# Kernel optimization log

Hardware: AMD Instinct MI355X
Metric: run time of the kernel (lower is better)

## Reference

```python
import jax, jax.numpy as jnp
import numpy as np

VOCAB = 50000
EMB = 300
HID = 300
LAYERS = 2
NTAGS = 11  # tags 0..8 are real labels, 9=START, 10=STOP
START = NTAGS - 2
STOP = NTAGS - 1
NEG = -10000.0


def _lstm_params(key, in_dim, hid):
    k = 1.0 / np.sqrt(hid)
    ks = jax.random.split(key, 4)
    u = lambda kk, shp: jax.random.uniform(kk, shp, jnp.float32, -k, k)
    return {
        'Wi': u(ks[0], (4 * hid, in_dim)),
        'Wh': u(ks[1], (4 * hid, hid)),
        'bi': u(ks[2], (4 * hid,)),
        'bh': u(ks[3], (4 * hid,)),
    }


def _run_lstm(p, xs, reverse=False):
    # xs: [T, B, D] -> [T, B, H]
    B = xs.shape[1]
    H = p['Wh'].shape[1]
    pre = jnp.einsum('tbd,gd->tbg', xs, p['Wi']) + p['bi'] + p['bh']

    def step(carry, pre_t):
        h, c = carry
        g = pre_t + h @ p['Wh'].T
        i, f, gg, o = jnp.split(g, 4, axis=-1)
        i = jax.nn.sigmoid(i)
        f = jax.nn.sigmoid(f)
        gg = jnp.tanh(gg)
        o = jax.nn.sigmoid(o)
        c = f * c + i * gg
        h = o * jnp.tanh(c)
        return (h, c), h

    init = (jnp.zeros((B, H), xs.dtype), jnp.zeros((B, H), xs.dtype))
    _, hs = jax.lax.scan(step, init, pre, reverse=reverse)
    return hs


def setup_inputs() -> dict:
    key = jax.random.key(0)
    ks = jax.random.split(key, 12)
    x = jax.random.randint(ks[0], (64, 512), 0, VOCAB, dtype=jnp.int32)
    emb = jax.random.normal(ks[1], (VOCAB, EMB), jnp.float32) * 0.02
    lstm = []
    ki = 2
    for layer in range(LAYERS):
        in_dim = EMB if layer == 0 else 2 * HID
        fwd = _lstm_params(ks[ki], in_dim, HID); ki += 1
        bwd = _lstm_params(ks[ki], in_dim, HID); ki += 1
        lstm.append((fwd, bwd))
    Wout = jax.random.normal(ks[ki], (NTAGS, 2 * HID), jnp.float32) * 0.02
    bout = jnp.zeros((NTAGS,), jnp.float32)
    trans = jax.random.normal(ks[ki + 1], (NTAGS, NTAGS), jnp.float32) * 0.1
    # transitions[i, j] = score of transitioning TO i FROM j
    trans = trans.at[START, :].set(NEG).at[:, STOP].set(NEG)
    params = {'emb': emb, 'Wout': Wout, 'bout': bout, 'trans': trans}
    for li, (f, b) in enumerate(lstm):
        for nm, d in (('f', f), ('b', b)):
            for k2, v in d.items():
                params[f'l{li}{nm}_{k2}'] = v
    return {'x': x, **params}


def _features(x, params):
    h = params['emb'][x]  # [B,T,E]
    h = jnp.transpose(h, (1, 0, 2))  # [T,B,E]
    for li in range(LAYERS):
        pf = {k2: params[f'l{li}f_{k2}'] for k2 in ('Wi', 'Wh', 'bi', 'bh')}
        pb = {k2: params[f'l{li}b_{k2}'] for k2 in ('Wi', 'Wh', 'bi', 'bh')}
        hf = _run_lstm(pf, h)
        hb = _run_lstm(pb, h, reverse=True)
        h = jnp.concatenate([hf, hb], axis=-1)  # [T,B,2H]
    feats = jnp.einsum('tbh,gh->tbg', h, params['Wout']) + params['bout']
    return feats  # [T,B,NTAGS]


def _viterbi(feats, trans):
    # feats: [T,B,K]; trans[i,j]: to i from j
    T, B, K = feats.shape
    init = jnp.full((B, K), NEG, feats.dtype).at[:, START].set(0.0)

    def step(fv, feat_t):
        # scores[b, i, j] = fv[b, j] + trans[i, j]
        scores = fv[:, None, :] + trans[None, :, :]
        bp = jnp.argmax(scores, axis=-1)  # [B,K]
        fv_new = jnp.max(scores, axis=-1) + feat_t
        return fv_new, bp

    fv, bps = jax.lax.scan(step, init, feats)  # bps: [T,B,K]
    term = fv + trans[STOP][None, :]
    best_last = jnp.argmax(term, axis=-1)  # [B]
    path_score = jnp.max(term, axis=-1)

    def back(tag, bp_t):
        prev = jnp.take_along_axis(bp_t, tag[:, None], axis=-1)[:, 0]
        return prev, tag

    _, path = jax.lax.scan(back, best_last, bps, reverse=True)  # [T,B]
    return path_score, jnp.transpose(path)  # [B], [B,T]


def reference(x, emb, Wout, bout, trans,
              l0f_Wi, l0f_Wh, l0f_bi, l0f_bh, l0b_Wi, l0b_Wh, l0b_bi, l0b_bh,
              l1f_Wi, l1f_Wh, l1f_bi, l1f_bh, l1b_Wi, l1b_Wh, l1b_bi, l1b_bh):
    params = dict(emb=emb, Wout=Wout, bout=bout, trans=trans,
                  l0f_Wi=l0f_Wi, l0f_Wh=l0f_Wh, l0f_bi=l0f_bi, l0f_bh=l0f_bh,
                  l0b_Wi=l0b_Wi, l0b_Wh=l0b_Wh, l0b_bi=l0b_bi, l0b_bh=l0b_bh,
                  l1f_Wi=l1f_Wi, l1f_Wh=l1f_Wh, l1f_bi=l1f_bi, l1f_bh=l1f_bh,
                  l1b_Wi=l1b_Wi, l1b_Wh=l1b_Wh, l1b_bi=l1b_bi, l1b_bh=l1b_bh)
    feats = _features(x, params)
    path_score, path = _viterbi(feats, trans)
    return path_score, path
```

## Files before the change

### kernel.cpp

```cpp
#include <hip/hip_runtime.h>
#include <hip/hip_bf16.h>

#define T_SEQ 512
#define NBATCH 64
#define HID 300
#define G4 1200
#define NTAG 11
#define TAG_START 9
#define TAG_STOP 10
#define NEGV -10000.0f
#define NWGD 38
#define NKT 10
#define HXE (40*2*64*8)
#define NPREW 150
#define FLGS 16
#define FLGN 152
#define FLGDIR (FLGN*FLGS)

typedef unsigned short u16;
using short8 = __attribute__((ext_vector_type(8))) short;
using f32x4  = __attribute__((ext_vector_type(4))) float;
using i32x4  = __attribute__((ext_vector_type(4))) int;

#define MF(a, b, c) __builtin_amdgcn_mfma_f32_16x16x32_bf16((a), (b), (c), 0, 0, 0)

__device__ __forceinline__ float sigf(float x) { return 1.0f / (1.0f + expf(-x)); }

__device__ __forceinline__ u16 f2bf(float x) {
    unsigned u = __float_as_uint(x);
    unsigned r = (u + 0x7FFFu + ((u >> 16) & 1u)) >> 16;
    return (u16)r;
}
__device__ __forceinline__ float bf2f(u16 h) {
    return __uint_as_float((unsigned)h << 16);
}

__device__ __forceinline__ i32x4 ld_cc_x4(const u16* p) {
    i32x4 r;
    asm volatile("global_load_dwordx4 %0, %1, off sc0 sc1" : "=v"(r) : "v"(p) : "memory");
    return r;
}
__device__ __forceinline__ unsigned ld_cc_b32(const unsigned* p) {
    unsigned r;
    asm volatile("global_load_dword %0, %1, off sc0 sc1\n\t"
                 "s_waitcnt vmcnt(0)" : "=v"(r) : "v"(p) : "memory");
    return r;
}
__device__ __forceinline__ void st_cc_x4(u16* p, i32x4 v) {
    asm volatile("global_store_dwordx4 %0, %1, off sc0 sc1" :: "v"(p), "v"(v) : "memory");
}
__device__ __forceinline__ void st_cc_b32(unsigned* p, unsigned v) {
    asm volatile("global_store_dword %0, %1, off sc0 sc1" :: "v"(p), "v"(v) : "memory");
}
__device__ __forceinline__ void wait_vm0() {
    asm volatile("s_waitcnt vmcnt(0)" ::: "memory");
}

__global__ __launch_bounds__(256) void k_gather(const int* __restrict__ x,
                                                const float* __restrict__ emb,
                                                u16* __restrict__ xs0)
{
    int t = blockIdx.x;
    __shared__ int rid[NBATCH];
    if (threadIdx.x < NBATCH) rid[threadIdx.x] = x[threadIdx.x * T_SEQ + t];
    __syncthreads();
    for (int o = threadIdx.x; o < 64 * 40; o += 256) {
        int b = o / 40, m8 = o - b * 40;
        unsigned hw[4], lw[4];
#pragma unroll
        for (int p = 0; p < 4; ++p) {
            int k0 = m8 * 8 + p * 2;
            float v0 = (k0 < 300)     ? emb[(size_t)rid[b] * 300 + k0]     : 0.0f;
            float v1 = (k0 + 1 < 300) ? emb[(size_t)rid[b] * 300 + k0 + 1] : 0.0f;
            u16 h0 = f2bf(v0), h1 = f2bf(v1);
            u16 l0 = f2bf(v0 - bf2f(h0)), l1 = f2bf(v1 - bf2f(h1));
            hw[p] = (unsigned)h0 | ((unsigned)h1 << 16);
            lw[p] = (unsigned)l0 | ((unsigned)l1 << 16);
        }
        u16* dst = xs0 + (((size_t)t * 40 + m8) * 64 + b) * 16;
        *(i32x4*)dst       = i32x4{(int)hw[0], (int)hw[1], (int)hw[2], (int)hw[3]};
        *(i32x4*)(dst + 8) = i32x4{(int)lw[0], (int)lw[1], (int)lw[2], (int)lw[3]};
    }
}

__global__ __launch_bounds__(256) void k_zpad(u16* __restrict__ xs1)
{
    int t = blockIdx.x;
    i32x4* base = (i32x4*)(xs1 + (((size_t)t * 80 + 76) * 64) * 16);
    i32x4 z = {0, 0, 0, 0};
    for (int o = threadIdx.x; o < 4 * 64 * 2; o += 256) base[o] = z;
}

template<int KT, int KMAX>
__device__ __forceinline__ void pregemm_role(
    const u16* __restrict__ xs,
    const float* __restrict__ Wi, const float* __restrict__ bi, const float* __restrict__ bh,
    float* __restrict__ pre, int jtile, int dir, int t0f, int t0b, int s0, int s1, int tid)
{
    int w = tid >> 6, l = tid & 63;
    int hh = l >> 4, kbx = l >> 4;
    int jj = jtile * 4 + hh;
    int bcol = w * 16 + (l & 15);

    short8 aH[KT], aL[KT];
    {
        int r = l & 15;
        int g = r & 3, uo = r >> 2;
        const float* wr = Wi + ((size_t)g * 300 + jtile * 4 + uo) * KMAX;
        int kb0 = kbx * 8;
#pragma unroll
        for (int kt = 0; kt < KT; ++kt) {
            short8 vh, vl;
#pragma unroll
            for (int e = 0; e < 8; ++e) {
                int kp = kt * 32 + kb0 + e;
                bool valid; int cc;
                if (KMAX == 600) { valid = (kp < 300) || (kp >= 304 && kp < 604); cc = (kp < 300) ? kp : kp - 4; }
                else             { valid = (kp < 300); cc = kp; }
                float wv = valid ? wr[cc] : 0.0f;
                u16 hb = f2bf(wv);
                vh[e] = (short)hb;
                vl[e] = (short)f2bf(wv - bf2f(hb));
            }
            aH[kt] = vh; aL[kt] = vl;
        }
    }
    float bias[4];
#pragma unroll
    for (int q = 0; q < 4; ++q) bias[q] = bi[q * 300 + jj] + bh[q * 300 + jj];

    const int NB8 = KT * 4;
    for (int s = s0; s < s1; ++s) {
        int t = dir ? (t0b - s) : (t0f + s);
        f32x4 a0 = {0.f,0.f,0.f,0.f}, a1 = {0.f,0.f,0.f,0.f}, a2 = {0.f,0.f,0.f,0.f};
#pragma unroll
        for (int kt = 0; kt < KT; ++kt) {
            const u16* gx = xs + (((size_t)t * NB8 + (4 * kt + kbx)) * 64 + bcol) * 16;
            short8 bhv = *(const short8*)gx;
            short8 blv = *(const short8*)(gx + 8);
            a0 = MF(aH[kt], bhv, a0);
            a1 = MF(aL[kt], bhv, a1);
            a2 = MF(aH[kt], blv, a2);
        }
#pragma unroll
        for (int q = 0; q < 4; ++q)
            pre[((size_t)s * G4 + q * 300 + jj) * 64 + bcol] = a0[q] + a1[q] + a2[q] + bias[q];
    }
}

template<int KT, int KMAX>
__global__ __launch_bounds__(256) void k_pregemm(
    const u16* __restrict__ xs,
    const float* __restrict__ WiF, const float* __restrict__ WiB,
    const float* __restrict__ biF, const float* __restrict__ bhF,
    const float* __restrict__ biB, const float* __restrict__ bhB,
    float* __restrict__ preF, float* __restrict__ preB,
    int t0f, int t0b, int NSL, int C)
{
    int bx = blockIdx.x;
    int idx = bx / (2 * NSL);
    int rem = bx - idx * 2 * NSL;
    int sl = rem >> 1, dir = rem & 1;
    int s0 = sl * 32, s1 = min(s0 + 32, C);
    pregemm_role<KT, KMAX>(xs,
        dir ? WiB : WiF, dir ? biB : biF, dir ? bhB : bhF,
        dir ? preB : preF, idx, dir, t0f, t0b, s0, s1, threadIdx.x);
}

template<int MODE>
__device__ __forceinline__ void lstm_role(
    const float* __restrict__ preF, const float* __restrict__ preB,
    const float* __restrict__ WhF, const float* __restrict__ WhB,
    u16* __restrict__ hx, float* __restrict__ cbuf,
    float* __restrict__ xs2, u16* __restrict__ xs1,
    int t0f, int t0b, int C, int first,
    unsigned* __restrict__ flags,
    volatile unsigned* wgprog,
    int bid, int tid)
{
    __builtin_amdgcn_s_setprio(1);
    int dir = bid & 1, idx = bid >> 1;
    const float* pre = dir ? preB : preF;
    const float* Wh  = dir ? WhB : WhF;
    u16* hxd = hx + (size_t)dir * 2 * HXE;
    float* cb = cbuf + (size_t)dir * 300 * 64;
    unsigned* flg = flags + (size_t)dir * FLGDIR;
    int w = tid >> 6, l = tid & 63;
    int hh = l >> 4, kbx = l >> 4;
    int bcol = w * 16 + (l & 15);
    int j0 = idx * 8;
    int ju0 = j0 + hh, ju1 = j0 + 4 + hh;
    int jc0 = min(ju0, 299), jc1 = min(ju1, 299);
    bool jv0 = ju0 < 300, jv1 = ju1 < 300;

    unsigned* myflag = flg + (size_t)(idx * 4 + w) * FLGS;
    const unsigned* shardp = flg + (size_t)(w * 38 + min(l, 37)) * FLGS;
    bool shact = l < 38;

    if (l == 0) wgprog[w] = 0;
    __syncthreads();

    short8 aH[2][NKT], aL[2][NKT];
    {
        int r = l & 15;
        int g = r & 3, uo = r >> 2;
#pragma unroll
        for (int q = 0; q < 2; ++q) {
            int jr = j0 + q * 4 + uo;
            const float* wr = Wh + ((size_t)g * 300 + min(jr, 299)) * 300;
            bool jvr = jr < 300;
#pragma unroll
            for (int kt = 0; kt < NKT; ++kt) {
                short8 vh, vl;
#pragma unroll
                for (int e = 0; e < 8; ++e) {
                    int k = kt * 32 + kbx * 8 + e;
                    float wv = (jvr && k < 300) ? wr[k] : 0.0f;
                    u16 hb = f2bf(wv);
                    vh[e] = (short)hb;
                    vl[e] = (short)f2bf(wv - bf2f(hb));
                }
                aH[q][kt] = vh; aL[q][kt] = vl;
            }
        }
    }
    float c0 = first ? 0.0f : cb[(size_t)jc0 * 64 + bcol];
    float c1 = first ? 0.0f : cb[(size_t)jc1 * 64 + bcol];

    float p0[4], p1[4];
#pragma unroll
    for (int g = 0; g < 4; ++g) {
        p0[g] = pre[((size_t)g * 300 + jc0) * 64 + bcol];
        p1[g] = pre[((size_t)g * 300 + jc1) * 64 + bcol];
    }

    int pp = 0;
    for (int s = 0; s < C; ++s) {
        f32x4 aA0 = {0.f,0.f,0.f,0.f}, aB0 = {0.f,0.f,0.f,0.f}, aC0 = {0.f,0.f,0.f,0.f};
        f32x4 aA1 = {0.f,0.f,0.f,0.f}, aB1 = {0.f,0.f,0.f,0.f}, aC1 = {0.f,0.f,0.f,0.f};
        if (!(first && s == 0)) {
            const u16* hxr = hxd + (size_t)pp * HXE;
            i32x4 bh[NKT], bl[NKT];
#pragma unroll
            for (int kt = 0; kt < NKT; ++kt) {
                const u16* gp = hxr + (size_t)(4 * kt + kbx) * 1024 + (size_t)bcol * 8;
                bh[kt] = ld_cc_x4(gp);
            }
#pragma unroll
            for (int kt = 0; kt < NKT; ++kt) {
                const u16* gp = hxr + (size_t)(4 * kt + kbx) * 1024 + (size_t)bcol * 8;
                bl[kt] = ld_cc_x4(gp + 512);
            }
            asm volatile("s_waitcnt vmcnt(10)" ::: "memory");
            __builtin_amdgcn_sched_barrier(0);
#pragma unroll
            for (int kt = 0; kt < NKT; ++kt) {
                short8 bhv = __builtin_bit_cast(short8, bh[kt]);
                aA0 = MF(aH[0][kt], bhv, aA0);
                aB0 = MF(aL[0][kt], bhv, aB0);
                aA1 = MF(aH[1][kt], bhv, aA1);
                aB1 = MF(aL[1][kt], bhv, aB1);
            }
            wait_vm0();
            __builtin_amdgcn_sched_barrier(0);
#pragma unroll
            for (int kt = 0; kt < NKT; ++kt) {
                short8 blv = __builtin_bit_cast(short8, bl[kt]);
                aC0 = MF(aH[0][kt], blv, aC0);
                aC1 = MF(aH[1][kt], blv, aC1);
            }
        }
        float hv0, hv1;
        {
            float gi = sigf(aA0[0] + aB0[0] + aC0[0] + p0[0]);
            float gf = sigf(aA0[1] + aB0[1] + aC0[1] + p0[1]);
            float gg = tanhf(aA0[2] + aB0[2] + aC0[2] + p0[2]);
            float go = sigf(aA0[3] + aB0[3] + aC0[3] + p0[3]);
            c0 = gf * c0 + gi * gg;
            hv0 = go * tanhf(c0);
            if (!jv0) hv0 = 0.0f;
        }
        {
            float gi = sigf(aA1[0] + aB1[0] + aC1[0] + p1[0]);
            float gf = sigf(aA1[1] + aB1[1] + aC1[1] + p1[1]);
            float gg = tanhf(aA1[2] + aB1[2] + aC1[2] + p1[2]);
            float go = sigf(aA1[3] + aB1[3] + aC1[3] + p1[3]);
            c1 = gf * c1 + gi * gg;
            hv1 = go * tanhf(c1);
            if (!jv1) hv1 = 0.0f;
        }
        u16 hb0 = f2bf(hv0);
        unsigned pk0 = (unsigned)hb0 | ((unsigned)f2bf(hv0 - bf2f(hb0)) << 16);
        u16 hb1 = f2bf(hv1);
        unsigned pk1 = (unsigned)hb1 | ((unsigned)f2bf(hv1 - bf2f(hb1)) << 16);
        int ls = l & 15;
        unsigned a0 = __shfl(pk0, ls), a1 = __shfl(pk0, ls + 16), a2 = __shfl(pk0, ls + 32), a3 = __shfl(pk0, ls + 48);
        unsigned b0 = __shfl(pk1, ls), b1 = __shfl(pk1, ls + 16), b2 = __shfl(pk1, ls + 32), b3 = __shfl(pk1, ls + 48);
        i32x4 hi4 = {(int)((a0 & 0xffffu) | (a1 << 16)), (int)((a2 & 0xffffu) | (a3 << 16)),
                     (int)((b0 & 0xffffu) | (b1 << 16)), (int)((b2 & 0xffffu) | (b3 << 16))};
        i32x4 lo4 = {(int)((a0 >> 16) | (a1 & 0xffff0000u)), (int)((a2 >> 16) | (a3 & 0xffff0000u)),
                     (int)((b0 >> 16) | (b1 & 0xffff0000u)), (int)((b2 >> 16) | (b3 & 0xffff0000u))};
        int t = dir ? (t0b - s) : (t0f + s);
        if (l < 16) {
            int b = w * 16 + l;
            u16* hxw = hxd + (size_t)(pp ^ 1) * HXE + (size_t)idx * 1024 + (size_t)b * 8;
            st_cc_x4(hxw, hi4);
            st_cc_x4(hxw + 512, lo4);
        }
        wait_vm0();
        if (l == 0) st_cc_b32(myflag, (unsigned)(s + 1));
        if (MODE == 0) {
            if (jv0) xs2[((size_t)t * 600 + dir * 300 + ju0) * 64 + bcol] = hv0;
            if (jv1) xs2[((size_t)t * 600 + dir * 300 + ju1) * 64 + bcol] = hv1;
        } else if (l < 16) {
            int b = w * 16 + l;
            u16* xd = xs1 + (((size_t)t * 80 + dir * 38 + idx) * 64 + b) * 16;
            *(i32x4*)xd       = hi4;
            *(i32x4*)(xd + 8) = lo4;
        }
        if (s + 1 < C) {
#pragma unroll
            for (int g = 0; g < 4; ++g) {
                p0[g] = pre[((size_t)(s + 1) * G4 + (size_t)g * 300 + jc0) * 64 + bcol];
                p1[g] = pre[((size_t)(s + 1) * G4 + (size_t)g * 300 + jc1) * 64 + bcol];
            }
            unsigned tgt = (unsigned)(s + 1);
            unsigned ok;
            do {
                unsigned v = tgt;
                if (shact) v = ld_cc_b32(shardp);
                ok = (v >= tgt) ? 1u : 0u;
            } while (!__all(ok));
            if (l == 0) wgprog[w] = tgt;
            while (!(wgprog[0] >= tgt && wgprog[1] >= tgt &&
                     wgprog[2] >= tgt && wgprog[3] >= tgt)) {
                __builtin_amdgcn_s_sleep(1);
            }
        }
        pp ^= 1;
    }
    if (jv0) cb[(size_t)jc0 * 64 + bcol] = c0;
    if (jv1) cb[(size_t)jc1 * 64 + bcol] = c1;
}

template<int KT, int KMAX, int MODE>
__global__ __launch_bounds__(256, 1) void k_chunk(
    const u16* __restrict__ xsN,
    const float* __restrict__ WiF, const float* __restrict__ WiB,
    const float* __restrict__ biF, const float* __restrict__ bhF,
    const float* __restrict__ biB, const float* __restrict__ bhB,
    float* __restrict__ preNF, float* __restrict__ preNB,
    int t0fN, int t0bN, int do_pre, int CN,
    const float* __restrict__ preF, const float* __restrict__ preB,
    const float* __restrict__ WhF, const float* __restrict__ WhB,
    u16* __restrict__ hx, float* __restrict__ cbuf,
    float* __restrict__ xs2, u16* __restrict__ xs1,
    int t0f, int t0b, int C, int first,
    unsigned* __restrict__ flags)
{
    __shared__ unsigned wgprog[4];
    int bid = blockIdx.x;
    if (bid < 2 * NWGD) {
        lstm_role<MODE>(preF, preB, WhF, WhB, hx, cbuf, xs2, xs1,
                        t0f, t0b, C, first, flags, wgprog, bid, threadIdx.x);
    } else if (do_pre) {
        int wg = bid - 2 * NWGD;
        int jtile = wg >> 1, dir = wg & 1;
        pregemm_role<KT, KMAX>(xsN,
            dir ? WiB : WiF, dir ? biB : biF, dir ? bhB : bhF,
            dir ? preNB : preNF, jtile, dir, t0fN, t0bN, 0, CN, threadIdx.x);
    }
}

__global__ __launch_bounds__(256) void k_feats(
    const float* __restrict__ xs2, const float* __restrict__ Wout,
    const float* __restrict__ bout, float* __restrict__ feats)
{
    int t = blockIdx.x;
    int tid = threadIdx.x;
    int b = tid & 63, g0 = tid >> 6;
    const float* xa = xs2 + (size_t)t * 600 * 64 + b;
    for (int g = g0; g < NTAG; g += 4) {
        float acc = bout[g];
        const float* wr = Wout + (size_t)g * 600;
#pragma unroll 4
        for (int k = 0; k < 600; ++k) acc += wr[k] * xa[(size_t)k * 64];
        feats[((size_t)t * NTAG + g) * 64 + b] = acc;
    }
}

__global__ __launch_bounds__(256) void k_viterbi(
    const float* __restrict__ feats, const float* __restrict__ trans,
    float* __restrict__ out)
{
    __shared__ unsigned char bp[4][T_SEQ * NTAG];
    int tid = threadIdx.x;
    int wv = tid >> 6, lane = tid & 63;
    int b = blockIdx.x * 4 + wv;
    int i = (lane < NTAG) ? lane : 0;
    bool act = lane < NTAG;
    float trow[NTAG];
#pragma unroll
    for (int j = 0; j < NTAG; ++j) trow[j] = trans[i * NTAG + j];
    float fv = (lane == TAG_START) ? 0.0f : NEGV;
    for (int t = 0; t < T_SEQ; ++t) {
        float m = -3.0e38f; int arg = 0;
#pragma unroll
        for (int j = 0; j < NTAG; ++j) {
            float fvj = __shfl(fv, j, 64);
            float sc = fvj + trow[j];
            if (sc > m) { m = sc; arg = j; }
        }
        float ft = feats[((size_t)t * NTAG + i) * 64 + b];
        fv = m + ft;
        if (act) bp[wv][t * NTAG + lane] = (unsigned char)arg;
    }
    float term = act ? (fv + trans[TAG_STOP * NTAG + i]) : -3.0e38f;
    int bi_ = lane;
#pragma unroll
    for (int off = 32; off >= 1; off >>= 1) {
        float ov = __shfl_xor(term, off, 64);
        int oi = __shfl_xor(bi_, off, 64);
        if (ov > term || (ov == term && oi < bi_)) { term = ov; bi_ = oi; }
    }
    if (lane == 0) {
        out[b] = term;
        int tag = bi_;
        float* po = out + 64 + (size_t)b * T_SEQ;
        for (int t = T_SEQ - 1; t >= 0; --t) {
            po[t] = (float)tag;
            tag = bp[wv][t * NTAG + tag];
        }
    }
}

extern "C" void kernel_launch(void* const* d_in, const int* in_sizes, int n_in,
                              void* d_out, int out_size, void* d_ws, size_t ws_size,
                              hipStream_t stream)
{
    (void)in_sizes; (void)n_in; (void)out_size;
    const int*   x     = (const int*)d_in[0];
    const float* emb   = (const float*)d_in[1];
    const float* Wout  = (const float*)d_in[2];
    const float* bout  = (const float*)d_in[3];
    const float* trans = (const float*)d_in[4];

    float* ws = (float*)d_ws;
    const size_t XS2F = (size_t)T_SEQ * 600 * NBATCH;
    const size_t XS1U = (size_t)T_SEQ * 80 * 64 * 16;
    const size_t FEA  = (size_t)T_SEQ * NTAG * NBATCH;

    float* xs2 = ws;
    u16* xs0 = (u16*)ws;
    u16* xs1 = (u16*)(ws + XS2F);
    float* featB = (float*)(xs1 + XS1U);
    float* cB = featB + FEA;
    u16* hxB = (u16*)(cB + 2 * 300 * 64);
    unsigned* flagsB = (unsigned*)(hxB + 4 * HXE);
    unsigned* padB = flagsB + 64ULL * 2 * FLGDIR;
    float* preBase = (float*)(padB + 16);
    size_t fixedBytes = (size_t)((char*)preBase - (char*)ws);

    int Cmax = 512;
    while (Cmax > 16 && fixedBytes + 4ULL * Cmax * G4 * NBATCH * 4ULL > ws_size) Cmax >>= 1;
    size_t slotF = 2ULL * Cmax * G4 * NBATCH;
    float* preS[2] = { preBase, preBase + slotF };

    int sizes[40], off[41], nch = 0;
    {
        int rem = T_SEQ;
        int f = (Cmax >= 64) ? 32 : Cmax;
        sizes[nch++] = f; rem -= f;
        while (rem > 0) { int s = rem < Cmax ? rem : Cmax; sizes[nch++] = s; rem -= s; }
        off[0] = 0;
        for (int i = 0; i < nch; ++i) off[i + 1] = off[i] + sizes[i];
    }

    (void)hipMemsetAsync(hxB, 0,
        4 * HXE * sizeof(u16) + (64ULL * 2 * FLGDIR) * sizeof(unsigned), stream);
    k_gather<<<T_SEQ, 256, 0, stream>>>(x, emb, xs0);
    k_zpad<<<T_SEQ, 256, 0, stream>>>(xs1);

    for (int layer = 0; layer < 2; ++layer) {
        int base = 5 + layer * 8;
        const float* WiF = (const float*)d_in[base + 0];
        const float* WhF = (const float*)d_in[base + 1];
        const float* biF = (const float*)d_in[base + 2];
        const float* bhF = (const float*)d_in[base + 3];
        const float* WiB = (const float*)d_in[base + 4];
        const float* WhB = (const float*)d_in[base + 5];
        const float* biB = (const float*)d_in[base + 6];
        const float* bhB = (const float*)d_in[base + 7];

        int NSL0 = (sizes[0] + 31) / 32;
        if (layer == 0)
            k_pregemm<10, 300><<<75 * 2 * NSL0, 256, 0, stream>>>(
                xs0, WiF, WiB, biF, bhF, biB, bhB,
                preS[0], preS[0] + slotF / 2, 0, T_SEQ - 1, NSL0, sizes[0]);
        else
            k_pregemm<20, 600><<<75 * 2 * NSL0, 256, 0, stream>>>(
                xs1, WiF, WiB, biF, bhF, biB, bhB,
                preS[0], preS[0] + slotF / 2, 0, T_SEQ - 1, NSL0, sizes[0]);

        for (int ci = 0; ci < nch; ++ci) {
            int cur = ci & 1, nxt = cur ^ 1;
            int t0f = off[ci], t0b = (T_SEQ - 1) - off[ci];
            int do_pre = (ci + 1 < nch) ? 1 : 0;
            int CN = do_pre ? sizes[ci + 1] : 0;
            int t0fN = off[ci + 1], t0bN = (T_SEQ - 1) - off[ci + 1];
            int slot = layer * 32 + ci;
            unsigned* flags = flagsB + (size_t)slot * 2 * FLGDIR;
            if (layer == 0)
                k_chunk<10, 300, 1><<<2 * NWGD + NPREW, 256, 0, stream>>>(
                    xs0, WiF, WiB, biF, bhF, biB, bhB,
                    preS[nxt], preS[nxt] + slotF / 2, t0fN, t0bN, do_pre, CN,
                    preS[cur], preS[cur] + slotF / 2, WhF, WhB, hxB, cB,
                    xs2, xs1, t0f, t0b, sizes[ci], (ci == 0) ? 1 : 0, flags);
            else
                k_chunk<20, 600, 0><<<2 * NWGD + NPREW, 256, 0, stream>>>(
                    xs1, WiF, WiB, biF, bhF, biB, bhB,
                    preS[nxt], preS[nxt] + slotF / 2, t0fN, t0bN, do_pre, CN,
                    preS[cur], preS[cur] + slotF / 2, WhF, WhB, hxB, cB,
                    xs2, xs1, t0f, t0b, sizes[ci], (ci == 0) ? 1 : 0, flags);
        }
    }
    k_feats<<<T_SEQ, 256, 0, stream>>>(xs2, Wout, bout, featB);
    k_viterbi<<<16, 256, 0, stream>>>(featB, trans, (float*)d_out);
}
```

Before: 5.896 ms.

## Halve recurrent LSTM workgroups, give each 16 hidden units, keep low-bf16 weights in LDS

Each direction's recurrent LSTM now runs on 19 workgroups instead of 38, and each workgroup owns 16 hidden units instead of 8. The high bf16 half of the recurrent weights stays in registers, while the low half moves into a 40KB LDS buffer that the MFMA loop reads each step. This cuts the number of workgroups that take part in the per-timestep cross-workgroup flag synchronisation and frees compute units for the overlapped pre-GEMM. In exchange each workgroup does twice the MFMA and activation work per step, and LDS reads are added to the critical path.

```diff
diff --git a/kernel.cpp b/kernel.cpp
--- a/kernel.cpp
+++ b/kernel.cpp
@@ -9,12 +9,12 @@
 #define TAG_START 9
 #define TAG_STOP 10
 #define NEGV -10000.0f
-#define NWGD 38
+#define NWGD 19
 #define NKT 10
 #define HXE (40*2*64*8)
 #define NPREW 150
 #define FLGS 16
-#define FLGN 152
+#define FLGN 76
 #define FLGDIR (FLGN*FLGS)
 
 typedef unsigned short u16;
@@ -175,7 +175,7 @@
     float* __restrict__ xs2, u16* __restrict__ xs1,
     int t0f, int t0b, int C, int first,
     unsigned* __restrict__ flags,
-    volatile unsigned* wgprog,
+    char* __restrict__ alo, volatile unsigned* wgprog,
     int bid, int tid)
 {
     __builtin_amdgcn_s_setprio(1);
@@ -188,24 +188,27 @@
     int w = tid >> 6, l = tid & 63;
     int hh = l >> 4, kbx = l >> 4;
     int bcol = w * 16 + (l & 15);
-    int j0 = idx * 8;
-    int ju0 = j0 + hh, ju1 = j0 + 4 + hh;
-    int jc0 = min(ju0, 299), jc1 = min(ju1, 299);
-    bool jv0 = ju0 < 300, jv1 = ju1 < 300;
+    int j0 = idx * 16;
+    int blk0 = idx * 2, blk1 = idx * 2 + 1;
+
+    int ju[4], jc[4]; bool jv[4];
+#pragma unroll
+    for (int q = 0; q < 4; ++q) {
+        ju[q] = j0 + q * 4 + hh;
+        jc[q] = min(ju[q], 299);
+        jv[q] = ju[q] < 300;
+    }
 
     unsigned* myflag = flg + (size_t)(idx * 4 + w) * FLGS;
-    const unsigned* shardp = flg + (size_t)(w * 38 + min(l, 37)) * FLGS;
-    bool shact = l < 38;
-
-    if (l == 0) wgprog[w] = 0;
-    __syncthreads();
-
-    short8 aH[2][NKT], aL[2][NKT];
+    const unsigned* shardp = flg + (size_t)(w * 19 + min(l, 18)) * FLGS;
+    bool shact = l < 19;
+
+    short8 aH[4][NKT];
     {
         int r = l & 15;
         int g = r & 3, uo = r >> 2;
 #pragma unroll
-        for (int q = 0; q < 2; ++q) {
+        for (int q = 0; q < 4; ++q) {
             int jr = j0 + q * 4 + uo;
             const float* wr = Wh + ((size_t)g * 300 + min(jr, 299)) * 300;
             bool jvr = jr < 300;
@@ -220,24 +223,30 @@
                     vh[e] = (short)hb;
                     vl[e] = (short)f2bf(wv - bf2f(hb));
                 }
-                aH[q][kt] = vh; aL[q][kt] = vl;
-            }
-        }
-    }
-    float c0 = first ? 0.0f : cb[(size_t)jc0 * 64 + bcol];
-    float c1 = first ? 0.0f : cb[(size_t)jc1 * 64 + bcol];
-
-    float p0[4], p1[4];
-#pragma unroll
-    for (int g = 0; g < 4; ++g) {
-        p0[g] = pre[((size_t)g * 300 + jc0) * 64 + bcol];
-        p1[g] = pre[((size_t)g * 300 + jc1) * 64 + bcol];
-    }
+                aH[q][kt] = vh;
+                if (q == w)
+                    *(short8*)(alo + ((size_t)(q * NKT + kt) * 1024) + (size_t)l * 16) = vl;
+            }
+        }
+    }
+    if (l == 0) wgprog[w] = 0;
+    __syncthreads();
+
+    float c[4];
+#pragma unroll
+    for (int q = 0; q < 4; ++q) c[q] = first ? 0.0f : cb[(size_t)jc[q] * 64 + bcol];
+
+    float p[4][4];
+#pragma unroll
+    for (int q = 0; q < 4; ++q)
+#pragma unroll
+        for (int g = 0; g < 4; ++g)
+            p[q][g] = pre[((size_t)g * 300 + jc[q]) * 64 + bcol];
 
     int pp = 0;
     for (int s = 0; s < C; ++s) {
-        f32x4 aA0 = {0.f,0.f,0.f,0.f}, aB0 = {0.f,0.f,0.f,0.f}, aC0 = {0.f,0.f,0.f,0.f};
-        f32x4 aA1 = {0.f,0.f,0.f,0.f}, aB1 = {0.f,0.f,0.f,0.f}, aC1 = {0.f,0.f,0.f,0.f};
+        f32x4 z = {0.f,0.f,0.f,0.f};
+        f32x4 aA[4] = {z, z, z, z}, aB[4] = {z, z, z, z}, aC[4] = {z, z, z, z};
         if (!(first && s == 0)) {
             const u16* hxr = hxd + (size_t)pp * HXE;
             i32x4 bh[NKT], bl[NKT];
@@ -256,74 +265,79 @@
 #pragma unroll
             for (int kt = 0; kt < NKT; ++kt) {
                 short8 bhv = __builtin_bit_cast(short8, bh[kt]);
-                aA0 = MF(aH[0][kt], bhv, aA0);
-                aB0 = MF(aL[0][kt], bhv, aB0);
-                aA1 = MF(aH[1][kt], bhv, aA1);
-                aB1 = MF(aL[1][kt], bhv, aB1);
+#pragma unroll
+                for (int q = 0; q < 4; ++q)
+                    aA[q] = MF(aH[q][kt], bhv, aA[q]);
+#pragma unroll
+                for (int q = 0; q < 4; ++q) {
+                    short8 alv = *(const short8*)(alo + ((size_t)(q * NKT + kt) * 1024) + (size_t)l * 16);
+                    aB[q] = MF(alv, bhv, aB[q]);
+                }
             }
             wait_vm0();
             __builtin_amdgcn_sched_barrier(0);
 #pragma unroll
             for (int kt = 0; kt < NKT; ++kt) {
                 short8 blv = __builtin_bit_cast(short8, bl[kt]);
-                aC0 = MF(aH[0][kt], blv, aC0);
-                aC1 = MF(aH[1][kt], blv, aC1);
-            }
-        }
-        float hv0, hv1;
-        {
-            float gi = sigf(aA0[0] + aB0[0] + aC0[0] + p0[0]);
-            float gf = sigf(aA0[1] + aB0[1] + aC0[1] + p0[1]);
-            float gg = tanhf(aA0[2] + aB0[2] + aC0[2] + p0[2]);
-            float go = sigf(aA0[3] + aB0[3] + aC0[3] + p0[3]);
-            c0 = gf * c0 + gi * gg;
-            hv0 = go * tanhf(c0);
-            if (!jv0) hv0 = 0.0f;
-        }
-        {
-            float gi = sigf(aA1[0] + aB1[0] + aC1[0] + p1[0]);
-            float gf = sigf(aA1[1] + aB1[1] + aC1[1] + p1[1]);
-            float gg = tanhf(aA1[2] + aB1[2] + aC1[2] + p1[2]);
-            float go = sigf(aA1[3] + aB1[3] + aC1[3] + p1[3]);
-            c1 = gf * c1 + gi * gg;
-            hv1 = go * tanhf(c1);
-            if (!jv1) hv1 = 0.0f;
-        }
-        u16 hb0 = f2bf(hv0);
-        unsigned pk0 = (unsigned)hb0 | ((unsigned)f2bf(hv0 - bf2f(hb0)) << 16);
-        u16 hb1 = f2bf(hv1);
-        unsigned pk1 = (unsigned)hb1 | ((unsigned)f2bf(hv1 - bf2f(hb1)) << 16);
+#pragma unroll
+                for (int q = 0; q < 4; ++q)
+                    aC[q] = MF(aH[q][kt], blv, aC[q]);
+            }
+        }
+        float hv[4]; unsigned pk[4];
+#pragma unroll
+        for (int q = 0; q < 4; ++q) {
+            float gi = sigf(aA[q][0] + aB[q][0] + aC[q][0] + p[q][0]);
+            float gf = sigf(aA[q][1] + aB[q][1] + aC[q][1] + p[q][1]);
+            float gg = tanhf(aA[q][2] + aB[q][2] + aC[q][2] + p[q][2]);
+            float go = sigf(aA[q][3] + aB[q][3] + aC[q][3] + p[q][3]);
+            c[q] = gf * c[q] + gi * gg;
+            float h = go * tanhf(c[q]);
+            if (!jv[q]) h = 0.0f;
+            hv[q] = h;
+            u16 hb = f2bf(h);
+            pk[q] = (unsigned)hb | ((unsigned)f2bf(h - bf2f(hb)) << 16);
+        }
         int ls = l & 15;
-        unsigned a0 = __shfl(pk0, ls), a1 = __shfl(pk0, ls + 16), a2 = __shfl(pk0, ls + 32), a3 = __shfl(pk0, ls + 48);
-        unsigned b0 = __shfl(pk1, ls), b1 = __shfl(pk1, ls + 16), b2 = __shfl(pk1, ls + 32), b3 = __shfl(pk1, ls + 48);
-        i32x4 hi4 = {(int)((a0 & 0xffffu) | (a1 << 16)), (int)((a2 & 0xffffu) | (a3 << 16)),
-                     (int)((b0 & 0xffffu) | (b1 << 16)), (int)((b2 & 0xffffu) | (b3 << 16))};
-        i32x4 lo4 = {(int)((a0 >> 16) | (a1 & 0xffff0000u)), (int)((a2 >> 16) | (a3 & 0xffff0000u)),
-                     (int)((b0 >> 16) | (b1 & 0xffff0000u)), (int)((b2 >> 16) | (b3 & 0xffff0000u))};
+        unsigned q0a = __shfl(pk[0], ls), q0b = __shfl(pk[0], ls + 16), q0c = __shfl(pk[0], ls + 32), q0d = __shfl(pk[0], ls + 48);
+        unsigned q1a = __shfl(pk[1], ls), q1b = __shfl(pk[1], ls + 16), q1c = __shfl(pk[1], ls + 32), q1d = __shfl(pk[1], ls + 48);
+        unsigned q2a = __shfl(pk[2], ls), q2b = __shfl(pk[2], ls + 16), q2c = __shfl(pk[2], ls + 32), q2d = __shfl(pk[2], ls + 48);
+        unsigned q3a = __shfl(pk[3], ls), q3b = __shfl(pk[3], ls + 16), q3c = __shfl(pk[3], ls + 32), q3d = __shfl(pk[3], ls + 48);
+        i32x4 hi4_0 = {(int)((q0a & 0xffffu) | (q0b << 16)), (int)((q0c & 0xffffu) | (q0d << 16)),
+                       (int)((q1a & 0xffffu) | (q1b << 16)), (int)((q1c & 0xffffu) | (q1d << 16))};
+        i32x4 lo4_0 = {(int)((q0a >> 16) | (q0b & 0xffff0000u)), (int)((q0c >> 16) | (q0d & 0xffff0000u)),
+                       (int)((q1a >> 16) | (q1b & 0xffff0000u)), (int)((q1c >> 16) | (q1d & 0xffff0000u))};
+        i32x4 hi4_1 = {(int)((q2a & 0xffffu) | (q2b << 16)), (int)((q2c & 0xffffu) | (q2d << 16)),
+                       (int)((q3a & 0xffffu) | (q3b << 16)), (int)((q3c & 0xffffu) | (q3d << 16))};
+        i32x4 lo4_1 = {(int)((q2a >> 16) | (q2b & 0xffff0000u)), (int)((q2c >> 16) | (q2d & 0xffff0000u)),
+                       (int)((q3a >> 16) | (q3b & 0xffff0000u)), (int)((q3c >> 16) | (q3d & 0xffff0000u))};
         int t = dir ? (t0b - s) : (t0f + s);
-        if (l < 16) {
-            int b = w * 16 + l;
-            u16* hxw = hxd + (size_t)(pp ^ 1) * HXE + (size_t)idx * 1024 + (size_t)b * 8;
-            st_cc_x4(hxw, hi4);
-            st_cc_x4(hxw + 512, lo4);
+        i32x4 h4 = (l < 16) ? hi4_0 : hi4_1;
+        i32x4 l4 = (l < 16) ? lo4_0 : lo4_1;
+        int blkS = (l < 16) ? blk0 : blk1;
+        int bb = w * 16 + ls;
+        if (l < 32) {
+            u16* hxw = hxd + (size_t)(pp ^ 1) * HXE + (size_t)blkS * 1024 + (size_t)bb * 8;
+            st_cc_x4(hxw, h4);
+            st_cc_x4(hxw + 512, l4);
         }
         wait_vm0();
         if (l == 0) st_cc_b32(myflag, (unsigned)(s + 1));
         if (MODE == 0) {
-            if (jv0) xs2[((size_t)t * 600 + dir * 300 + ju0) * 64 + bcol] = hv0;
-            if (jv1) xs2[((size_t)t * 600 + dir * 300 + ju1) * 64 + bcol] = hv1;
-        } else if (l < 16) {
-            int b = w * 16 + l;
-            u16* xd = xs1 + (((size_t)t * 80 + dir * 38 + idx) * 64 + b) * 16;
-            *(i32x4*)xd       = hi4;
-            *(i32x4*)(xd + 8) = lo4;
+#pragma unroll
+            for (int q = 0; q < 4; ++q)
+                if (jv[q]) xs2[((size_t)t * 600 + dir * 300 + ju[q]) * 64 + bcol] = hv[q];
+        } else if (l < 32) {
+            u16* xd = xs1 + (((size_t)t * 80 + dir * 38 + blkS) * 64 + bb) * 16;
+            *(i32x4*)xd       = h4;
+            *(i32x4*)(xd + 8) = l4;
         }
         if (s + 1 < C) {
 #pragma unroll
-            for (int g = 0; g < 4; ++g) {
-                p0[g] = pre[((size_t)(s + 1) * G4 + (size_t)g * 300 + jc0) * 64 + bcol];
-                p1[g] = pre[((size_t)(s + 1) * G4 + (size_t)g * 300 + jc1) * 64 + bcol];
-            }
+            for (int q = 0; q < 4; ++q)
+#pragma unroll
+                for (int g = 0; g < 4; ++g)
+                    p[q][g] = pre[((size_t)(s + 1) * G4 + (size_t)g * 300 + jc[q]) * 64 + bcol];
             unsigned tgt = (unsigned)(s + 1);
             unsigned ok;
             do {
@@ -339,8 +353,9 @@
         }
         pp ^= 1;
     }
-    if (jv0) cb[(size_t)jc0 * 64 + bcol] = c0;
-    if (jv1) cb[(size_t)jc1 * 64 + bcol] = c1;
+#pragma unroll
+    for (int q = 0; q < 4; ++q)
+        if (jv[q]) cb[(size_t)jc[q] * 64 + bcol] = c[q];
 }
 
 template<int KT, int KMAX, int MODE>
@@ -358,11 +373,13 @@
     int t0f, int t0b, int C, int first,
     unsigned* __restrict__ flags)
 {
-    __shared__ unsigned wgprog[4];
+    __shared__ __align__(16) char smem[40 * 1024 + 64];
     int bid = blockIdx.x;
     if (bid < 2 * NWGD) {
         lstm_role<MODE>(preF, preB, WhF, WhB, hx, cbuf, xs2, xs1,
-                        t0f, t0b, C, first, flags, wgprog, bid, threadIdx.x);
+                        t0f, t0b, C, first, flags,
+                        smem, (volatile unsigned*)(smem + 40 * 1024),
+                        bid, threadIdx.x);
     } else if (do_pre) {
         int wg = bid - 2 * NWGD;
         int jtile = wg >> 1, dir = wg & 1;
```

Measured after the change: 7.197 ms. 22.1% more time.

## Split next-chunk input GEMM out of LSTM chunk kernel into separate launch

Applied to the files above, without the earlier changes.

Removes the extra pre-GEMM workgroups that ran alongside the recurrent LSTM workgroups in k_chunk, and instead launches k_pregemm as a separate kernel after each chunk. This undoes the overlap of the next chunk's input projection with the current chunk's recurrence. The aim is to stop the pre-GEMM blocks from competing with the latency-critical recurrent blocks for CUs, cache and memory bandwidth. The cost is that the projection work becomes serialized between chunks.

```diff
diff --git a/kernel.cpp b/kernel.cpp
--- a/kernel.cpp
+++ b/kernel.cpp
@@ -12,7 +12,6 @@
 #define NWGD 38
 #define NKT 10
 #define HXE (40*2*64*8)
-#define NPREW 150
 #define FLGS 16
 #define FLGN 152
 #define FLGDIR (FLGN*FLGS)
@@ -343,14 +342,8 @@
     if (jv1) cb[(size_t)jc1 * 64 + bcol] = c1;
 }
 
-template<int KT, int KMAX, int MODE>
+template<int MODE>
 __global__ __launch_bounds__(256, 1) void k_chunk(
-    const u16* __restrict__ xsN,
-    const float* __restrict__ WiF, const float* __restrict__ WiB,
-    const float* __restrict__ biF, const float* __restrict__ bhF,
-    const float* __restrict__ biB, const float* __restrict__ bhB,
-    float* __restrict__ preNF, float* __restrict__ preNB,
-    int t0fN, int t0bN, int do_pre, int CN,
     const float* __restrict__ preF, const float* __restrict__ preB,
     const float* __restrict__ WhF, const float* __restrict__ WhB,
     u16* __restrict__ hx, float* __restrict__ cbuf,
@@ -359,17 +352,8 @@
     unsigned* __restrict__ flags)
 {
     __shared__ unsigned wgprog[4];
-    int bid = blockIdx.x;
-    if (bid < 2 * NWGD) {
-        lstm_role<MODE>(preF, preB, WhF, WhB, hx, cbuf, xs2, xs1,
-                        t0f, t0b, C, first, flags, wgprog, bid, threadIdx.x);
-    } else if (do_pre) {
-        int wg = bid - 2 * NWGD;
-        int jtile = wg >> 1, dir = wg & 1;
-        pregemm_role<KT, KMAX>(xsN,
-            dir ? WiB : WiF, dir ? biB : biF, dir ? bhB : bhF,
-            dir ? preNB : preNF, jtile, dir, t0fN, t0bN, 0, CN, threadIdx.x);
-    }
+    lstm_role<MODE>(preF, preB, WhF, WhB, hx, cbuf, xs2, xs1,
+                    t0f, t0b, C, first, flags, wgprog, blockIdx.x, threadIdx.x);
 }
 
 __global__ __launch_bounds__(256) void k_feats(
@@ -505,23 +489,30 @@
         for (int ci = 0; ci < nch; ++ci) {
             int cur = ci & 1, nxt = cur ^ 1;
             int t0f = off[ci], t0b = (T_SEQ - 1) - off[ci];
-            int do_pre = (ci + 1 < nch) ? 1 : 0;
-            int CN = do_pre ? sizes[ci + 1] : 0;
-            int t0fN = off[ci + 1], t0bN = (T_SEQ - 1) - off[ci + 1];
             int slot = layer * 32 + ci;
             unsigned* flags = flagsB + (size_t)slot * 2 * FLGDIR;
             if (layer == 0)
-                k_chunk<10, 300, 1><<<2 * NWGD + NPREW, 256, 0, stream>>>(
-                    xs0, WiF, WiB, biF, bhF, biB, bhB,
-                    preS[nxt], preS[nxt] + slotF / 2, t0fN, t0bN, do_pre, CN,
+                k_chunk<1><<<2 * NWGD, 256, 0, stream>>>(
                     preS[cur], preS[cur] + slotF / 2, WhF, WhB, hxB, cB,
                     xs2, xs1, t0f, t0b, sizes[ci], (ci == 0) ? 1 : 0, flags);
             else
-                k_chunk<20, 600, 0><<<2 * NWGD + NPREW, 256, 0, stream>>>(
-                    xs1, WiF, WiB, biF, bhF, biB, bhB,
-                    preS[nxt], preS[nxt] + slotF / 2, t0fN, t0bN, do_pre, CN,
+                k_chunk<0><<<2 * NWGD, 256, 0, stream>>>(
                     preS[cur], preS[cur] + slotF / 2, WhF, WhB, hxB, cB,
                     xs2, xs1, t0f, t0b, sizes[ci], (ci == 0) ? 1 : 0, flags);
+
+            if (ci + 1 < nch) {
+                int CN = sizes[ci + 1];
+                int NSLn = (CN + 31) / 32;
+                int t0fN = off[ci + 1], t0bN = (T_SEQ - 1) - off[ci + 1];
+                if (layer == 0)
+                    k_pregemm<10, 300><<<75 * 2 * NSLn, 256, 0, stream>>>(
+                        xs0, WiF, WiB, biF, bhF, biB, bhB,
+                        preS[nxt], preS[nxt] + slotF / 2, t0fN, t0bN, NSLn, CN);
+                else
+                    k_pregemm<20, 600><<<75 * 2 * NSLn, 256, 0, stream>>>(
+                        xs1, WiF, WiB, biF, bhF, biB, bhB,
+                        preS[nxt], preS[nxt] + slotF / 2, t0fN, t0bN, NSLn, CN);
+            }
         }
     }
     k_feats<<<T_SEQ, 256, 0, stream>>>(xs2, Wout, bout, featB);
```

Result: slower. 8.343 ms (+41.5%).
